# Kernel tuning notes

Hardware: AMD Instinct MI355X
Metric: run time of the kernel (lower is better)

## Reference

```python
import jax, jax.numpy as jnp
import numpy as np

B, C, N_ELEM = 16, 256, 8192
N_FILT, N_DIL = 2, 256


def setup_inputs() -> dict:
    key = jax.random.key(0)
    kx, kw = jax.random.split(key)
    x = jax.random.normal(kx, (B, C, N_ELEM), dtype=jnp.float32)
    # xavier_uniform on a (n_out, n_in, n_filt) tensor: fan_in = fan_out = C * N_FILT
    fan = C * N_FILT
    bound = float(np.sqrt(6.0 / (fan + fan)))
    weight = jax.random.uniform(kw, (C, C, N_FILT), minval=-bound, maxval=bound, dtype=jnp.float32)
    return {"x": x, "weight": weight, "n_dil": N_DIL}


def reference(x, weight, n_dil):
    # x: (B, C_in, N); weight: (C_out, C_in, n_filt); requires C_out == C_in.
    n_out, n_in, n_filt = weight.shape
    filter_size = (n_filt - 1) * n_dil + 1
    n_steps = x.shape[2] - filter_size

    # The torch loop computes, for i in [0, n_steps):
    #   x[:, :, i+1] = sum_{c,k} weight[o, c, k] * x_read[:, c, i + k*n_dil]
    # where the k=0 tap reads the UPDATED x (written at step i-1) and all
    # k>=1 taps read the ORIGINAL x (those positions are written at later
    # steps, and torch evaluates the conv before the in-place write).
    # => affine recurrence: s[i+1] = W0 @ s[i] + c[i], s[0] = x[:, :, 0].

    # c[t] = sum_{k>=1} W_k @ x_orig[:, :, t + k*n_dil]  -> (n_steps, B, C_out)
    c = jnp.zeros((n_steps, x.shape[0], n_out), dtype=x.dtype)
    for k in range(1, n_filt):
        xk = x[:, :, k * n_dil: k * n_dil + n_steps]  # (B, C_in, n_steps)
        c = c + jnp.einsum('oc,bct->tbo', weight[:, :, k], xk)

    W0T = weight[:, :, 0].T  # (C_in, C_out)

    def step(state, ct):
        # state: (B, C); ct: (B, C)
        new = state @ W0T + ct
        return new, new

    _, ys = jax.lax.scan(step, x[:, :, 0], c)  # ys: (n_steps, B, C)
    x_out = x.at[:, :, 1:1 + n_steps].set(jnp.transpose(ys, (1, 2, 0)))
    return x_out
```

## Files before the change

kernel.cpp:

```cpp
#include <hip/hip_runtime.h>
#include <stdint.h>


constexpr int BATCH  = 16;
constexpr int CH     = 256;
constexpr int NEL    = 8192;
constexpr int NDIL   = 256;
constexpr int TSTEPS = NEL - (NDIL + 1);
constexpr int LCH    = 16;
constexpr int NCH    = (TSTEPS + LCH - 1) / LCH;
constexpr int OUT_L  = 32;
constexpr int WARM   = 20;
constexpr int NCH2   = (TSTEPS + OUT_L - 1) / OUT_L;
constexpr int TPB    = 256;
constexpr int YPAD   = 260;
constexpr int A2PAD  = 264;
constexpr int TTILES = (TSTEPS + 127) / 128;
constexpr int YROW   = 264;

constexpr size_t OFF_AF    = 0;
constexpr size_t OFF_P1    = OFF_AF    + 256 * 1024;
constexpr size_t OFF_P2    = OFF_P1    + 256 * 1024;
constexpr size_t OFF_AB16  = OFF_P2    + 256 * 1024;
constexpr size_t OFF_W1B   = OFF_AB16  + 128 * 1024;
constexpr size_t OFF_E     = OFF_W1B   + 128 * 1024;
constexpr size_t OFF_INIT  = OFF_E     + (size_t)NCH * BATCH * CH * 4;
constexpr size_t OFF_AFRAG = OFF_INIT  + (size_t)(NCH + 1) * BATCH * CH * 4;
constexpr size_t OFF_W1FR  = OFF_AFRAG + 128 * 1024;
constexpr size_t OFF_CBUF  = OFF_W1FR  + 128 * 1024;
constexpr size_t CBUF_BYTES = (size_t)(NCH * LCH) * BATCH * CH * 2;
constexpr size_t OFF_YBUF  = OFF_CBUF + CBUF_BYTES;
constexpr size_t WS_NEED   = OFF_YBUF + CBUF_BYTES;

typedef __attribute__((ext_vector_type(8))) short bf16x8;
typedef __attribute__((ext_vector_type(4))) float f32x4;

__device__ __forceinline__ float bfu(uint32_t hibits) { return __uint_as_float(hibits); }
__device__ __forceinline__ float bf2f(uint16_t b) { return __uint_as_float(((uint32_t)b) << 16); }
__device__ __forceinline__ uint16_t f2bf(float f) {
  uint32_t u = __float_as_uint(f);
  uint32_t r = u + 0x7fffu + ((u >> 16) & 1u);
  return (uint16_t)(r >> 16);
}

__global__ void k_prep(const float* __restrict__ w, float* __restrict__ Af,
                       uint16_t* __restrict__ Ab, uint16_t* __restrict__ W1b,
                       uint16_t* __restrict__ Afrag, uint16_t* __restrict__ W1f) {
  int o = blockIdx.x, c = threadIdx.x;
  const float2 wv = *(const float2*)&w[(size_t)(o * CH + c) * 2];
  Af[c * CH + o]  = wv.x;
  Ab[c * CH + o]  = f2bf(wv.x);
  W1b[c * CH + o] = f2bf(wv.y);
  if (Afrag) {
    int kb = c >> 5, g = (c >> 3) & 3, ii = c & 7;
    int nt = o >> 4, mm = o & 15;
    size_t idx = (((size_t)(kb * 16 + nt) * 64) + (g * 16 + mm)) * 8 + ii;
    Afrag[idx] = f2bf(wv.x);
    W1f[idx]   = f2bf(wv.y);
  }
}

__global__ void k_init0(const float* __restrict__ x, float* __restrict__ initbuf) {
  int b = blockIdx.x, c = threadIdx.x;
  initbuf[b * CH + c] = x[(size_t)(b * CH + c) * NEL];
}

__global__ __launch_bounds__(TPB) void k_sqmm(const float* __restrict__ in,
                                              float* __restrict__ outm) {
  __shared__ __align__(16) float row[CH];
  int r = blockIdx.x, o = threadIdx.x;
  row[o] = in[r * CH + o];
  __syncthreads();
  float acc = 0.f;
#pragma unroll 8
  for (int k = 0; k < CH; ++k) acc += row[k] * in[k * CH + o];
  outm[r * CH + o] = acc;
}

__global__ void k_edges(const float* __restrict__ x, float* __restrict__ out) {
  size_t base = (size_t)blockIdx.x * NEL;
  int t = threadIdx.x;
  out[base + (NEL - 256) + t] = x[base + (NEL - 256) + t];
  if (t == 0) out[base] = x[base];
}

__global__ __launch_bounds__(512, 2) void k_cgemm_m(const float* __restrict__ x,
                                                    const uint16_t* __restrict__ W1f,
                                                    uint16_t* __restrict__ cb) {
  __shared__ __align__(16) uint16_t Axs[64 * 64 * 8];
  int tid = threadIdx.x, bid = blockIdx.x;
  int b = bid / TTILES, tt = bid % TTILES;
  int t0 = tt * 128;
  int w = tid >> 6, l = tid & 63, lm = l & 15, g = l >> 4;
  const float* xb = x + (size_t)b * CH * NEL + (t0 + NDIL);

  bf16x8 bv[8][2];
#pragma unroll
  for (int kb = 0; kb < 8; ++kb)
#pragma unroll
    for (int p = 0; p < 2; ++p)
      bv[kb][p] =
          *(const bf16x8*)&W1f[(((size_t)(kb * 16 + w * 2 + p) * 64) + l) * 8];

  int tA = w * 16 + lm;
  {
    float v[8][8];
#pragma unroll
    for (int k2 = 0; k2 < 8; ++k2)
#pragma unroll
      for (int i = 0; i < 8; ++i)
        v[k2][i] = xb[(size_t)(k2 * 32 + g * 8 + i) * NEL + tA];
#pragma unroll
    for (int k2 = 0; k2 < 8; ++k2) {
      uint4 pk;
      pk.x = (uint32_t)f2bf(v[k2][0]) | ((uint32_t)f2bf(v[k2][1]) << 16);
      pk.y = (uint32_t)f2bf(v[k2][2]) | ((uint32_t)f2bf(v[k2][3]) << 16);
      pk.z = (uint32_t)f2bf(v[k2][4]) | ((uint32_t)f2bf(v[k2][5]) << 16);
      pk.w = (uint32_t)f2bf(v[k2][6]) | ((uint32_t)f2bf(v[k2][7]) << 16);
      *(uint4*)&Axs[((w * 8 + k2) * 64 + l) * 8] = pk;
    }
  }
  __syncthreads();

#pragma unroll 1
  for (int mt = 0; mt < 8; ++mt) {
    f32x4 acc0 = (f32x4)0.f, acc1 = (f32x4)0.f;
#pragma unroll
    for (int kb = 0; kb < 8; ++kb) {
      bf16x8 av = *(const bf16x8*)&Axs[((mt * 8 + kb) * 64 + l) * 8];
      acc0 = __builtin_amdgcn_mfma_f32_16x16x32_bf16(av, bv[kb][0], acc0, 0, 0, 0);
      acc1 = __builtin_amdgcn_mfma_f32_16x16x32_bf16(av, bv[kb][1], acc1, 0, 0, 0);
    }
#pragma unroll
    for (int r = 0; r < 4; ++r) {
      int t2 = t0 + mt * 16 + g * 4 + r;
      if (t2 < TSTEPS) {
        size_t base = (size_t)t2 * (BATCH * CH) + b * CH;
        cb[base + (w * 2 + 0) * 16 + lm] = f2bf(acc0[r]);
        cb[base + (w * 2 + 1) * 16 + lm] = f2bf(acc1[r]);
      }
    }
  }
}

__device__ __forceinline__ void scan2_step(
    int t, bool pref, bool doout, const uint16_t* Yr, uint16_t* Yw,
    const uint16_t* __restrict__ cb, uint16_t* __restrict__ yb,
    const bf16x8 af[8][4], ushort* cc, int w, int lm, int g, int tid) {
  bf16x8 yv[8];
#pragma unroll
  for (int kb = 0; kb < 8; ++kb)
    yv[kb] = *(const bf16x8*)&Yr[lm * YROW + kb * 32 + g * 8];
  f32x4 acc[4];
#pragma unroll
  for (int ntl = 0; ntl < 4; ++ntl)
#pragma unroll
    for (int r = 0; r < 4; ++r)
      acc[ntl][r] = bfu(((uint32_t)cc[ntl * 4 + r]) << 16);
  if (pref) {
    size_t cbase = (size_t)(t + 2) * (BATCH * CH);
#pragma unroll
    for (int ntl = 0; ntl < 4; ++ntl)
#pragma unroll
      for (int r = 0; r < 4; ++r)
        cc[ntl * 4 + r] = cb[cbase + (g * 4 + r) * CH + (w * 4 + ntl) * 16 + lm];
  }
#pragma unroll
  for (int ntl = 0; ntl < 4; ++ntl) {
#pragma unroll
    for (int kb = 0; kb < 8; ++kb)
      acc[ntl] = __builtin_amdgcn_mfma_f32_16x16x32_bf16(yv[kb], af[kb][ntl], acc[ntl], 0, 0, 0);
  }
  uint16_t hbv[16];
#pragma unroll
  for (int ntl = 0; ntl < 4; ++ntl)
#pragma unroll
    for (int r = 0; r < 4; ++r) {
      float v = acc[ntl][r];
      int bb = g * 4 + r, o = (w * 4 + ntl) * 16 + lm;
      uint16_t hb = f2bf(v);
      hbv[ntl * 4 + r] = hb;
      Yw[bb * YROW + o] = hb;
    }
  if (doout) {
    uint4 p0, p1;
    p0.x = (uint32_t)hbv[0] | ((uint32_t)hbv[1] << 16);
    p0.y = (uint32_t)hbv[2] | ((uint32_t)hbv[3] << 16);
    p0.z = (uint32_t)hbv[4] | ((uint32_t)hbv[5] << 16);
    p0.w = (uint32_t)hbv[6] | ((uint32_t)hbv[7] << 16);
    p1.x = (uint32_t)hbv[8] | ((uint32_t)hbv[9] << 16);
    p1.y = (uint32_t)hbv[10] | ((uint32_t)hbv[11] << 16);
    p1.z = (uint32_t)hbv[12] | ((uint32_t)hbv[13] << 16);
    p1.w = (uint32_t)hbv[14] | ((uint32_t)hbv[15] << 16);
    uint4* dst = (uint4*)&yb[(size_t)t * 4096 + tid * 16];
    dst[0] = p0;
    dst[1] = p1;
  }
  asm volatile("s_waitcnt lgkmcnt(0)" ::: "memory");
  __builtin_amdgcn_sched_barrier(0);
  __builtin_amdgcn_s_barrier();
  __builtin_amdgcn_sched_barrier(0);
}

__global__ __launch_bounds__(TPB, 2) void k_scan2(
    const uint16_t* __restrict__ Afrag, const uint16_t* __restrict__ cb,
    uint16_t* __restrict__ yb, const float* __restrict__ x) {
  __shared__ __align__(16) uint16_t Y[2][16 * YROW];
  int tid = threadIdx.x;
  int j = blockIdx.x;
  int w = tid >> 6, l = tid & 63;
  int lm = l & 15, g = l >> 4;

  bf16x8 af[8][4];
#pragma unroll
  for (int kb = 0; kb < 8; ++kb)
#pragma unroll
    for (int ntl = 0; ntl < 4; ++ntl) {
      int nt = w * 4 + ntl;
      af[kb][ntl] = *(const bf16x8*)&Afrag[(((size_t)(kb * 16 + nt) * 64) + l) * 8];
    }

  int tstart   = (j == 0) ? 0 : OUT_L * j - WARM;
  int outstart = OUT_L * j;
  int tend     = min(OUT_L * (j + 1), TSTEPS);

  if (j == 0) {
    int b = tid >> 4, o0 = (tid & 15) * 16;
#pragma unroll
    for (int q = 0; q < 16; ++q)
      Y[0][b * YROW + o0 + q] = f2bf(x[(size_t)(b * CH + o0 + q) * NEL]);
  } else {
    for (int q = tid; q < 16 * YROW; q += TPB) Y[0][q] = 0;
  }

  ushort c0[16], c1[16];
  {
#pragma unroll
    for (int ntl = 0; ntl < 4; ++ntl)
#pragma unroll
      for (int r = 0; r < 4; ++r) {
        size_t off = (size_t)(g * 4 + r) * CH + (w * 4 + ntl) * 16 + lm;
        c0[ntl * 4 + r] = cb[(size_t)tstart * (BATCH * CH) + off];
        c1[ntl * 4 + r] = cb[(size_t)(tstart + 1) * (BATCH * CH) + off];
      }
  }
  __syncthreads();

#pragma unroll 1
  for (int ii = 0; ii < OUT_L + WARM + 2; ii += 2) {
    int t = tstart + ii;
    if (t >= tend) break;
    scan2_step(t, t + 2 < tend, t >= outstart, Y[0], Y[1], cb, yb,
               af, c0, w, lm, g, tid);
    if (t + 1 >= tend) break;
    scan2_step(t + 1, t + 3 < tend, t + 1 >= outstart, Y[1], Y[0], cb, yb,
               af, c1, w, lm, g, tid);
  }
}

__global__ __launch_bounds__(TPB) void k_yout(const uint16_t* __restrict__ yb,
                                              float* __restrict__ out) {
  __shared__ __align__(16) uint16_t t2[256 * 72];
  int bid = blockIdx.x;
  int tb = bid >> 4, sub = bid & 15;
  int G = sub >> 2, wS = sub & 3;
  int t0 = tb * 64;
  int tid = threadIdx.x;
  {
    int tl = tid >> 2, part = tid & 3;
    int ty = t0 + tl - 1;
    if (ty >= 0) {
      const uint16_t* src =
          &yb[(size_t)ty * 4096 + (wS * 64 + G * 16) * 16 + part * 64];
#pragma unroll
      for (int i = 0; i < 8; ++i) {
        uint4 vv = *(const uint4*)&src[i * 8];
        uint32_t uu[4] = {vv.x, vv.y, vv.z, vv.w};
        int colb = part * 64 + i * 8;
#pragma unroll
        for (int e = 0; e < 4; ++e) {
          t2[(colb + 2 * e) * 72 + tl]     = (uint16_t)(uu[e] & 0xffffu);
          t2[(colb + 2 * e + 1) * 72 + tl] = (uint16_t)(uu[e] >> 16);
        }
      }
    }
  }
  __syncthreads();
  {
    int b = G * 4 + (tid >> 6);
    int o = wS * 64 + (tid & 63);
    int col = (o & 15) * 16 + ((o >> 4) & 3) * 4 + (b & 3);
    float* dst = &out[(size_t)(b * CH + o) * NEL + t0];
#pragma unroll
    for (int k4 = 0; k4 < 4; ++k4) {
      uint4 v0 = *(const uint4*)&t2[col * 72 + k4 * 16];
      uint4 v1 = *(const uint4*)&t2[col * 72 + k4 * 16 + 8];
      uint32_t uu[8] = {v0.x, v0.y, v0.z, v0.w, v1.x, v1.y, v1.z, v1.w};
      float f[16];
#pragma unroll
      for (int e = 0; e < 8; ++e) {
        f[2 * e]     = bfu(uu[e] << 16);
        f[2 * e + 1] = bfu(uu[e] & 0xffff0000u);
      }
      if (tb == 0 && k4 == 0) {
#pragma unroll
        for (int e = 1; e < 16; ++e) dst[e] = f[e];
      } else {
#pragma unroll
        for (int m = 0; m < 4; ++m)
          *(float4*)&dst[k4 * 16 + m * 4] =
              make_float4(f[4 * m], f[4 * m + 1], f[4 * m + 2], f[4 * m + 3]);
      }
    }
  }
}

__global__ __launch_bounds__(TPB) void k_cgemm_v(const float* __restrict__ x,
                                                 const uint16_t* __restrict__ W1b,
                                                 float* __restrict__ out) {
  __shared__ __align__(16) uint16_t w1[CH * 128];
  __shared__ __align__(16) float xs[32][128];
  int tid = threadIdx.x;
  int bid = blockIdx.x;
  int b = bid / (TTILES * 2);
  int rem = bid % (TTILES * 2);
  int ttile = rem >> 1, otile = rem & 1;
  int t0 = ttile * 128, o0 = otile * 128;
  int tx = tid & 15, ty = tid >> 4;
  int o8 = o0 + tx * 8;
  int tb = t0 + ty * 8;
  {
    uint4* dst = (uint4*)w1;
    for (int q = tid; q < CH * 128 / 8; q += TPB) {
      int row = q >> 4, seg = q & 15;
      dst[q] = *(const uint4*)&W1b[row * CH + o0 + seg * 8];
    }
  }
  float acc[8][8];
#pragma unroll
  for (int i = 0; i < 8; ++i)
#pragma unroll
    for (int j = 0; j < 8; ++j) acc[i][j] = 0.f;
  for (int c0 = 0; c0 < CH; c0 += 32) {
    __syncthreads();
#pragma unroll
    for (int kk = 0; kk < 4; ++kk) {
      int q = tid + kk * TPB;
      int cc = q >> 5, tf = (q & 31) * 4;
      *(float4*)&xs[cc][tf] =
          *(const float4*)&x[(size_t)(b * CH + c0 + cc) * NEL + t0 + NDIL + tf];
    }
    __syncthreads();
#pragma unroll 4
    for (int cc = 0; cc < 32; ++cc) {
      float4 xa = *(const float4*)&xs[cc][ty * 8];
      float4 xb = *(const float4*)&xs[cc][ty * 8 + 4];
      float xv[8] = {xa.x, xa.y, xa.z, xa.w, xb.x, xb.y, xb.z, xb.w};
      uint4 wv = *(const uint4*)&w1[(c0 + cc) * 128 + tx * 8];
      float wf[8] = {bfu(wv.x << 16), bfu(wv.x & 0xffff0000u),
                     bfu(wv.y << 16), bfu(wv.y & 0xffff0000u),
                     bfu(wv.z << 16), bfu(wv.z & 0xffff0000u),
                     bfu(wv.w << 16), bfu(wv.w & 0xffff0000u)};
#pragma unroll
      for (int i = 0; i < 8; ++i)
#pragma unroll
        for (int j = 0; j < 8; ++j) acc[i][j] += xv[i] * wf[j];
    }
  }
#pragma unroll
  for (int j = 0; j < 8; ++j) {
    size_t base = (size_t)(b * CH + o8 + j) * NEL + tb + 1;
#pragma unroll
    for (int i = 0; i < 8; ++i)
      if (tb + i < TSTEPS) out[base + i] = acc[i][j];
  }
}

template <bool PH3>
__global__ __launch_bounds__(TPB) void k_scan(const uint16_t* __restrict__ Ab,
                                              const float* __restrict__ initbuf,
                                              float* __restrict__ Ebuf,
                                              float* __restrict__ out) {
  __shared__ __align__(16) uint16_t Al[CH * CH];
  __shared__ __align__(16) float yl[BATCH * YPAD];
  int tid = threadIdx.x;
  int j = blockIdx.x;
  {
    const uint4* src = (const uint4*)Ab;
    uint4* dst = (uint4*)Al;
    for (int q = tid; q < CH * CH / 8; q += TPB) dst[q] = src[q];
  }
  if constexpr (PH3) {
    for (int q = tid; q < BATCH * CH / 4; q += TPB) {
      int b = q >> 6, c4 = (q & 63) * 4;
      *(float4*)&yl[b * YPAD + c4] =
          *(const float4*)&initbuf[(size_t)j * BATCH * CH + b * CH + c4];
    }
  } else {
    for (int q = tid; q < BATCH * YPAD; q += TPB) yl[q] = 0.f;
  }
  __syncthreads();
  int o4 = (tid & 63) * 4;
  int b4 = (tid >> 6) * 4;
  int len = min(LCH, TSTEPS - j * LCH);
  float acc[4][4];
  for (int i = 0; i < len; ++i) {
    int t = j * LCH + i;
    float cv[4][4];
#pragma unroll
    for (int bb = 0; bb < 4; ++bb)
#pragma unroll
      for (int oo = 0; oo < 4; ++oo)
        cv[bb][oo] = out[(size_t)((b4 + bb) * CH + o4 + oo) * NEL + t + 1];
#pragma unroll
    for (int bb = 0; bb < 4; ++bb)
#pragma unroll
      for (int oo = 0; oo < 4; ++oo) acc[bb][oo] = 0.f;
#pragma unroll 2
    for (int c = 0; c < CH; c += 4) {
      float4 v0 = *(const float4*)&yl[(b4 + 0) * YPAD + c];
      float4 v1 = *(const float4*)&yl[(b4 + 1) * YPAD + c];
      float4 v2 = *(const float4*)&yl[(b4 + 2) * YPAD + c];
      float4 v3 = *(const float4*)&yl[(b4 + 3) * YPAD + c];
      float y0[4] = {v0.x, v0.y, v0.z, v0.w};
      float y1[4] = {v1.x, v1.y, v1.z, v1.w};
      float y2[4] = {v2.x, v2.y, v2.z, v2.w};
      float y3[4] = {v3.x, v3.y, v3.z, v3.w};
#pragma unroll
      for (int k = 0; k < 4; ++k) {
        uint2 au = *(const uint2*)&Al[(c + k) * CH + o4];
        float a[4] = {bfu(au.x << 16), bfu(au.x & 0xffff0000u),
                      bfu(au.y << 16), bfu(au.y & 0xffff0000u)};
#pragma unroll
        for (int oo = 0; oo < 4; ++oo) {
          acc[0][oo] += y0[k] * a[oo];
          acc[1][oo] += y1[k] * a[oo];
          acc[2][oo] += y2[k] * a[oo];
          acc[3][oo] += y3[k] * a[oo];
        }
      }
    }
#pragma unroll
    for (int bb = 0; bb < 4; ++bb)
#pragma unroll
      for (int oo = 0; oo < 4; ++oo) acc[bb][oo] += cv[bb][oo];
    __syncthreads();
#pragma unroll
    for (int bb = 0; bb < 4; ++bb)
      *(float4*)&yl[(b4 + bb) * YPAD + o4] =
          make_float4(acc[bb][0], acc[bb][1], acc[bb][2], acc[bb][3]);
    if constexpr (PH3) {
#pragma unroll
      for (int bb = 0; bb < 4; ++bb)
#pragma unroll
        for (int oo = 0; oo < 4; ++oo)
          out[(size_t)((b4 + bb) * CH + o4 + oo) * NEL + t + 1] = acc[bb][oo];
    }
    __syncthreads();
  }
  if constexpr (!PH3) {
#pragma unroll
    for (int bb = 0; bb < 4; ++bb)
#pragma unroll
      for (int oo = 0; oo < 4; ++oo)
        Ebuf[(size_t)j * BATCH * CH + (b4 + bb) * CH + o4 + oo] = acc[bb][oo];
  }
}

__global__ __launch_bounds__(TPB) void k_phase2(const float* __restrict__ ALf,
                                                const float* __restrict__ Ebuf,
                                                float* __restrict__ initbuf) {
  __shared__ __align__(16) uint16_t At[CH * A2PAD];
  __shared__ __align__(16) float st[CH];
  int b = blockIdx.x, tid = threadIdx.x;
  for (int q = tid; q < CH * CH; q += TPB) {
    int c = q >> 8, o = q & 255;
    At[o * A2PAD + c] = f2bf(ALf[q]);
  }
  st[tid] = initbuf[b * CH + tid];
  __syncthreads();
  for (int jj = 1; jj < NCH; ++jj) {
    float acc = Ebuf[(size_t)(jj - 1) * BATCH * CH + b * CH + tid];
#pragma unroll 4
    for (int c = 0; c < CH; c += 8) {
      uint4 au = *(const uint4*)&At[tid * A2PAD + c];
      float4 s0 = *(const float4*)&st[c];
      float4 s1 = *(const float4*)&st[c + 4];
      acc += bfu(au.x << 16) * s0.x + bfu(au.x & 0xffff0000u) * s0.y +
             bfu(au.y << 16) * s0.z + bfu(au.y & 0xffff0000u) * s0.w +
             bfu(au.z << 16) * s1.x + bfu(au.z & 0xffff0000u) * s1.y +
             bfu(au.w << 16) * s1.z + bfu(au.w & 0xffff0000u) * s1.w;
    }
    __syncthreads();
    st[tid] = acc;
    initbuf[(size_t)jj * BATCH * CH + b * CH + tid] = acc;
    __syncthreads();
  }
}

extern "C" void kernel_launch(void* const* d_in, const int* in_sizes, int n_in,
                              void* d_out, int out_size, void* d_ws, size_t ws_size,
                              hipStream_t stream) {
  const float* x = (const float*)d_in[0];
  const float* w = (const float*)d_in[1];
  float* out = (float*)d_out;
  char* ws = (char*)d_ws;

  float*    Af    = (float*)(ws + OFF_AF);
  float*    P1    = (float*)(ws + OFF_P1);
  float*    P2    = (float*)(ws + OFF_P2);
  uint16_t* Ab    = (uint16_t*)(ws + OFF_AB16);
  uint16_t* W1b   = (uint16_t*)(ws + OFF_W1B);
  float*    Ebuf  = (float*)(ws + OFF_E);
  float*    inb   = (float*)(ws + OFF_INIT);
  uint16_t* Afrag = (uint16_t*)(ws + OFF_AFRAG);
  uint16_t* W1f   = (uint16_t*)(ws + OFF_W1FR);
  uint16_t* cbuf  = (uint16_t*)(ws + OFF_CBUF);
  uint16_t* ybuf  = (uint16_t*)(ws + OFF_YBUF);

  const bool fast = ws_size >= WS_NEED;

  k_prep<<<CH, CH, 0, stream>>>(w, Af, Ab, W1b, fast ? Afrag : nullptr, W1f);
  if (fast) {
    k_edges<<<BATCH * CH, 256, 0, stream>>>(x, out);
    k_cgemm_m<<<BATCH * TTILES, 512, 0, stream>>>(x, W1f, cbuf);
    k_scan2<<<NCH2, TPB, 0, stream>>>(Afrag, cbuf, ybuf, x);
    k_yout<<<124 * 16, TPB, 0, stream>>>(ybuf, out);
  } else {
    k_edges<<<BATCH * CH, 256, 0, stream>>>(x, out);
    k_init0<<<BATCH, CH, 0, stream>>>(x, inb);
    k_sqmm<<<CH, TPB, 0, stream>>>(Af, P1);
    k_sqmm<<<CH, TPB, 0, stream>>>(P1, P2);
    k_sqmm<<<CH, TPB, 0, stream>>>(P2, P1);
    k_sqmm<<<CH, TPB, 0, stream>>>(P1, P2);
    k_cgemm_v<<<BATCH * TTILES * 2, TPB, 0, stream>>>(x, W1b, out);
    k_scan<false><<<NCH - 1, TPB, 0, stream>>>(Ab, nullptr, Ebuf, out);
    k_phase2<<<BATCH, TPB, 0, stream>>>(P2, Ebuf, inb);
    k_scan<true><<<NCH, TPB, 0, stream>>>(Ab, inb, nullptr, out);
  }
}
```

Measured before the change: 189.1 us.

## Vectorize x loads in c-GEMM with truncating bf16 packing and swizzled LDS

The c-GEMM kernel now loads x with 16-byte vector loads along time instead of scalar strided loads per channel. Pairs of channels are packed into bf16 words by truncating the fp32 values rather than rounding, and stored into an XOR-swizzled LDS layout. The time tile shrinks from 128 to 64, doubling the grid. The intent is to cut global-load instruction count and improve coalescing, at the cost of changed bf16 rounding (truncation) and more LDS reads per MFMA operand.

```diff
diff --git a/kernel.cpp b/kernel.cpp
--- a/kernel.cpp
+++ b/kernel.cpp
@@ -16,6 +16,7 @@
 constexpr int YPAD   = 260;
 constexpr int A2PAD  = 264;
 constexpr int TTILES = (TSTEPS + 127) / 128;
+constexpr int TT64   = 124;
 constexpr int YROW   = 264;
 
 constexpr size_t OFF_AF    = 0;
@@ -87,10 +88,10 @@
 __global__ __launch_bounds__(512, 2) void k_cgemm_m(const float* __restrict__ x,
                                                     const uint16_t* __restrict__ W1f,
                                                     uint16_t* __restrict__ cb) {
-  __shared__ __align__(16) uint16_t Axs[64 * 64 * 8];
+  __shared__ __align__(16) uint32_t Xs[128 * 64];
   int tid = threadIdx.x, bid = blockIdx.x;
-  int b = bid / TTILES, tt = bid % TTILES;
-  int t0 = tt * 128;
+  int b = bid / TT64, tt = bid % TT64;
+  int t0 = tt * 64;
   int w = tid >> 6, l = tid & 63, lm = l & 15, g = l >> 4;
   const float* xb = x + (size_t)b * CH * NEL + (t0 + NDIL);
 
@@ -102,32 +103,41 @@
       bv[kb][p] =
           *(const bf16x8*)&W1f[(((size_t)(kb * 16 + w * 2 + p) * 64) + l) * 8];
 
-  int tA = w * 16 + lm;
   {
-    float v[8][8];
-#pragma unroll
-    for (int k2 = 0; k2 < 8; ++k2)
-#pragma unroll
-      for (int i = 0; i < 8; ++i)
-        v[k2][i] = xb[(size_t)(k2 * 32 + g * 8 + i) * NEL + tA];
-#pragma unroll
-    for (int k2 = 0; k2 < 8; ++k2) {
-      uint4 pk;
-      pk.x = (uint32_t)f2bf(v[k2][0]) | ((uint32_t)f2bf(v[k2][1]) << 16);
-      pk.y = (uint32_t)f2bf(v[k2][2]) | ((uint32_t)f2bf(v[k2][3]) << 16);
-      pk.z = (uint32_t)f2bf(v[k2][4]) | ((uint32_t)f2bf(v[k2][5]) << 16);
-      pk.w = (uint32_t)f2bf(v[k2][6]) | ((uint32_t)f2bf(v[k2][7]) << 16);
-      *(uint4*)&Axs[((w * 8 + k2) * 64 + l) * 8] = pk;
+    int cp = tid >> 2, tq4 = tid & 3, gs = (tid >> 4) & 3;
+    const float* rl = xb + (size_t)(2 * cp) * NEL;
+    const float* rh = rl + NEL;
+    uint4 lo[4], hi[4];
+#pragma unroll
+    for (int a = 0; a < 4; ++a) {
+      lo[a] = *(const uint4*)&rl[(a * 4 + tq4) * 4];
+      hi[a] = *(const uint4*)&rh[(a * 4 + tq4) * 4];
+    }
+#pragma unroll
+    for (int a = 0; a < 4; ++a) {
+      int tq = a * 4 + tq4;
+      int slot = tq ^ (gs << 2);
+      uint4 d;
+      d.x = (hi[a].x & 0xffff0000u) | (lo[a].x >> 16);
+      d.y = (hi[a].y & 0xffff0000u) | (lo[a].y >> 16);
+      d.z = (hi[a].z & 0xffff0000u) | (lo[a].z >> 16);
+      d.w = (hi[a].w & 0xffff0000u) | (lo[a].w >> 16);
+      *(uint4*)&Xs[cp * 64 + slot * 4] = d;
     }
   }
   __syncthreads();
 
 #pragma unroll 1
-  for (int mt = 0; mt < 8; ++mt) {
+  for (int mt = 0; mt < 4; ++mt) {
+    int soff = (((mt * 4 + (lm >> 2)) ^ (g << 2)) << 2) + (lm & 3);
     f32x4 acc0 = (f32x4)0.f, acc1 = (f32x4)0.f;
 #pragma unroll
     for (int kb = 0; kb < 8; ++kb) {
-      bf16x8 av = *(const bf16x8*)&Axs[((mt * 8 + kb) * 64 + l) * 8];
+      bf16x8 av;
+      uint32_t* avp = (uint32_t*)&av;
+      int cpb = kb * 16 + g * 4;
+#pragma unroll
+      for (int j = 0; j < 4; ++j) avp[j] = Xs[(cpb + j) * 64 + soff];
       acc0 = __builtin_amdgcn_mfma_f32_16x16x32_bf16(av, bv[kb][0], acc0, 0, 0, 0);
       acc1 = __builtin_amdgcn_mfma_f32_16x16x32_bf16(av, bv[kb][1], acc1, 0, 0, 0);
     }
@@ -523,7 +533,7 @@
   k_prep<<<CH, CH, 0, stream>>>(w, Af, Ab, W1b, fast ? Afrag : nullptr, W1f);
   if (fast) {
     k_edges<<<BATCH * CH, 256, 0, stream>>>(x, out);
-    k_cgemm_m<<<BATCH * TTILES, 512, 0, stream>>>(x, W1f, cbuf);
+    k_cgemm_m<<<BATCH * TT64, 512, 0, stream>>>(x, W1f, cbuf);
     k_scan2<<<NCH2, TPB, 0, stream>>>(Afrag, cbuf, ybuf, x);
     k_yout<<<124 * 16, TPB, 0, stream>>>(ybuf, out);
   } else {
```

New measurement: 190.5 us. No clear change (+0.7%).
